# Optimization experiments

Hardware: AMD Instinct MI355X
Metric: run time of the kernel (lower is better)

Reference implementation:

```python
import jax, jax.numpy as jnp
import numpy as np

B, T, D = 4, 4096, 1024
F = 4 * D
EPS_INIT = -1e30  # log-space -inf surrogate for the stable WKV state


def layer_norm(x, w, b, eps=1e-5):
    mu = jnp.mean(x, axis=-1, keepdims=True)
    var = jnp.var(x, axis=-1, keepdims=True)
    return (x - mu) * jax.lax.rsqrt(var + eps) * w + b


def time_shift(x):
    # last_x[t] = x[t-1], zeros at t=0 (init_x buffer is zeros)
    return jnp.concatenate([jnp.zeros_like(x[:, :1]), x[:, :-1]], axis=1)


def wkv(w, u, k, v):
    """Numerically stable RWKV WKV recurrence.
    w, u: [D] (w already exponentiated decay rate); k, v: [B,T,D].
    Maintains (alpha, beta, eps) so that wkv_t = (sum_i e^{k_i - (t-1-i)w} v_i + e^{u+k_t} v_t)
                                               / (sum_i e^{k_i - (t-1-i)w}     + e^{u+k_t})."""
    bsz, _, dim = k.shape
    alpha0 = jnp.zeros((bsz, dim), k.dtype)
    beta0 = jnp.zeros((bsz, dim), k.dtype)
    eps0 = jnp.full((bsz, dim), EPS_INIT, k.dtype)

    def step(carry, kv_t):
        alpha, beta, eps = carry
        kt, vt = kv_t
        ukt = u + kt
        tau = jnp.maximum(ukt, eps)
        e1 = jnp.exp(eps - tau)
        e2 = jnp.exp(ukt - tau)
        out = (e1 * alpha + e2 * vt) / (e1 * beta + e2)
        # decay state by exp(-w) in log-space, then absorb k_t
        weps = eps - w
        tau2 = jnp.maximum(weps, kt)
        d1 = jnp.exp(weps - tau2)
        d2 = jnp.exp(kt - tau2)
        return (d1 * alpha + d2 * vt, d1 * beta + d2, tau2), out

    kT = jnp.swapaxes(k, 0, 1)  # [T,B,D]
    vT = jnp.swapaxes(v, 0, 1)
    _, outT = jax.lax.scan(step, (alpha0, beta0, eps0), (kT, vT))
    return jnp.swapaxes(outT, 0, 1)  # [B,T,D]


def setup_inputs() -> dict:
    key = jax.random.key(0)
    ks = jax.random.split(key, 20)
    n = lambda k, shape, s: jax.random.normal(k, shape, jnp.float32) * s
    u = lambda k, shape: jax.random.uniform(k, shape, jnp.float32)
    s = 0.02
    return {
        "x": jax.random.normal(ks[0], (B, T, D), jnp.float32),
        "ln1_w": jnp.ones((D,), jnp.float32), "ln1_b": jnp.zeros((D,), jnp.float32),
        "ln2_w": jnp.ones((D,), jnp.float32), "ln2_b": jnp.zeros((D,), jnp.float32),
        "time_decay": n(ks[1], (D,), 0.5),
        "time_first": n(ks[2], (D,), 0.5),
        "time_mix_k": u(ks[3], (1, 1, D)),
        "time_mix_v": u(ks[4], (1, 1, D)),
        "time_mix_r": u(ks[5], (1, 1, D)),
        "w_key": n(ks[6], (D, D), s),
        "w_value": n(ks[7], (D, D), s),
        "w_recept": n(ks[8], (D, D), s),
        "w_output": n(ks[9], (D, D), s),
        "f_time_mix_k": u(ks[10], (1, 1, D)),
        "f_time_mix_r": u(ks[11], (1, 1, D)),
        "f_w_key": n(ks[12], (D, F), s),
        "f_w_recept": n(ks[13], (D, D), s),
        "f_w_value": n(ks[14], (F, D), s),
    }


def reference(x, ln1_w, ln1_b, ln2_w, ln2_b,
              time_decay, time_first, time_mix_k, time_mix_v, time_mix_r,
              w_key, w_value, w_recept, w_output,
              f_time_mix_k, f_time_mix_r, f_w_key, f_w_recept, f_w_value):
    # --- attention (time-mix) sub-block ---
    xn = layer_norm(x, ln1_w, ln1_b)
    lx = time_shift(xn)
    k = (xn * time_mix_k + lx * (1.0 - time_mix_k)) @ w_key
    v = (xn * time_mix_v + lx * (1.0 - time_mix_v)) @ w_value
    r = (xn * time_mix_r + lx * (1.0 - time_mix_r)) @ w_recept
    sr = jax.nn.sigmoid(r)
    w = jnp.exp(time_decay)
    out = wkv(w, time_first, k, v)
    x = x + (out * sr) @ w_output
    # --- feed-forward (channel-mix) sub-block ---
    xn2 = layer_norm(x, ln2_w, ln2_b)
    lx2 = time_shift(xn2)
    fk = (xn2 * f_time_mix_k + lx2 * (1.0 - f_time_mix_k)) @ f_w_key
    fr = (xn2 * f_time_mix_r + lx2 * (1.0 - f_time_mix_r)) @ f_w_recept
    vk = jnp.square(jax.nn.relu(fk)) @ f_w_value
    x = x + jax.nn.sigmoid(fr) * vk
    return x
```

## Files before the change

kernel.cpp:

```cpp
#include <hip/hip_runtime.h>

#define DV 1024
#define TT 4096
#define BB 4
#define FF 4096
#define MM (BB*TT)
#define NCH 64
#define LCH 64

typedef __attribute__((ext_vector_type(8))) short bf16x8;
typedef __attribute__((ext_vector_type(4))) float f32x4;
typedef __attribute__((ext_vector_type(8))) unsigned short u16x8;
typedef __attribute__((ext_vector_type(4))) unsigned short u16x4;

__device__ __forceinline__ float bf2f(unsigned short h) {
    union { unsigned int u; float f; } c; c.u = ((unsigned int)h) << 16; return c.f;
}
__device__ __forceinline__ unsigned short f2bf(float f) {
    union { float f; unsigned int u; } c; c.f = f;
    unsigned int r = c.u + 0x7fffu + ((c.u >> 16) & 1u);
    return (unsigned short)(r >> 16);
}

__global__ void diag_kernel(float* out, float v) { out[0] = v; }

__global__ __launch_bounds__(256) void transpose_cast(
    const float* __restrict__ src, unsigned short* __restrict__ dst, int K, int N)
{
    __shared__ float t[32][33];
    int n0 = blockIdx.x * 32, k0 = blockIdx.y * 32;
    int tx = threadIdx.x, ty = threadIdx.y;
    #pragma unroll
    for (int i = 0; i < 4; ++i)
        t[ty*4+i][tx] = src[(size_t)(k0 + ty*4 + i) * N + n0 + tx];
    __syncthreads();
    #pragma unroll
    for (int i = 0; i < 4; ++i)
        dst[(size_t)(n0 + ty*4 + i) * K + k0 + tx] = f2bf(t[tx][ty*4+i]);
}

template<bool BF16IN>
__global__ __launch_bounds__(256) void ln_kernel(
    const void* __restrict__ xin, const float* __restrict__ w, const float* __restrict__ b,
    unsigned short* __restrict__ out)
{
    int row = blockIdx.x;
    int t = threadIdx.x;
    float v0, v1, v2, v3;
    if (BF16IN) {
        u16x4 h = *(const u16x4*)((const unsigned short*)xin + (size_t)row * DV + t * 4);
        v0 = bf2f(h[0]); v1 = bf2f(h[1]); v2 = bf2f(h[2]); v3 = bf2f(h[3]);
    } else {
        float4 v = ((const float4*)((const float*)xin + (size_t)row * DV))[t];
        v0 = v.x; v1 = v.y; v2 = v.z; v3 = v.w;
    }
    float s = v0 + v1 + v2 + v3;
    float q = v0*v0 + v1*v1 + v2*v2 + v3*v3;
    #pragma unroll
    for (int off = 32; off >= 1; off >>= 1) {
        s += __shfl_down(s, off);
        q += __shfl_down(q, off);
    }
    __shared__ float ss[4], qq[4];
    if ((t & 63) == 0) { ss[t >> 6] = s; qq[t >> 6] = q; }
    __syncthreads();
    s = ss[0] + ss[1] + ss[2] + ss[3];
    q = qq[0] + qq[1] + qq[2] + qq[3];
    float mu = s * (1.f/DV);
    float var = q * (1.f/DV) - mu*mu;
    float rs = rsqrtf(var + 1e-5f);
    int d = t * 4;
    u16x4 o;
    o[0] = f2bf((v0 - mu)*rs*w[d+0] + b[d+0]);
    o[1] = f2bf((v1 - mu)*rs*w[d+1] + b[d+1]);
    o[2] = f2bf((v2 - mu)*rs*w[d+2] + b[d+2]);
    o[3] = f2bf((v3 - mu)*rs*w[d+3] + b[d+3]);
    *(u16x4*)(out + (size_t)row*DV + d) = o;
}

__global__ __launch_bounds__(256) void mix_kernel(
    const unsigned short* __restrict__ xn,
    const float* __restrict__ ck, const float* __restrict__ cv, const float* __restrict__ cr,
    unsigned short* __restrict__ ok, unsigned short* __restrict__ ov, unsigned short* __restrict__ orr)
{
    int gid = blockIdx.x * 256 + threadIdx.x;
    int row = gid >> 7;
    int d0 = (gid & 127) << 3;
    size_t base = (size_t)row * DV + d0;
    u16x8 cur = *(const u16x8*)(xn + base);
    bool hp = (row & (TT - 1)) != 0;
    u16x8 prev = (u16x8)0;
    if (hp) prev = *(const u16x8*)(xn + base - DV);
    u16x8 rk, rv, rr2;
    #pragma unroll
    for (int e = 0; e < 8; ++e) {
        float xc = bf2f(cur[e]);
        float xp = hp ? bf2f(prev[e]) : 0.f;
        float a = ck[d0+e]; rk[e] = f2bf(xc*a + xp*(1.f-a));
        float bb = cv[d0+e]; rv[e] = f2bf(xc*bb + xp*(1.f-bb));
        if (orr) { float c = cr[d0+e]; rr2[e] = f2bf(xc*c + xp*(1.f-c)); }
    }
    *(u16x8*)(ok + base) = rk;
    *(u16x8*)(ov + base) = rv;
    if (orr) *(u16x8*)(orr + base) = rr2;
}


__global__ __launch_bounds__(256) void wkv_phase1(
    const unsigned short* __restrict__ k, const unsigned short* __restrict__ v,
    const float* __restrict__ time_decay,
    float* __restrict__ saP, float* __restrict__ sbP, float* __restrict__ mP)
{
    int gid = blockIdx.x * 256 + threadIdx.x;
    int d = gid & (DV - 1);
    int bc = gid >> 10;
    int b = bc >> 6, c = bc & (NCH - 1);
    float w = __expf(time_decay[d]);
    float alpha = 0.f, beta = 0.f, m = -1e30f;
    size_t base = ((size_t)b * TT + (size_t)c * LCH) * DV + d;
    for (int t = 0; t < LCH; ++t) {
        size_t idx = base + (size_t)t * DV;
        float kt = bf2f(k[idx]);
        float vt = bf2f(v[idx]);
        float wm = m - w;
        float tau = fmaxf(wm, kt);
        float d1 = __expf(wm - tau);
        float d2 = __expf(kt - tau);
        alpha = d1*alpha + d2*vt;
        beta  = d1*beta + d2;
        m = tau;
    }
    saP[gid] = alpha; sbP[gid] = beta; mP[gid] = m;
}

__global__ __launch_bounds__(256) void wkv_phase2(
    const float* __restrict__ time_decay,
    float* __restrict__ saP, float* __restrict__ sbP, float* __restrict__ mP)
{
    int gid = blockIdx.x * 256 + threadIdx.x;
    int b = gid >> 10, d = gid & (DV - 1);
    float Lw = (float)LCH * __expf(time_decay[d]);
    float A = 0.f, Bv = 0.f, E = -1e30f;
    for (int c = 0; c < NCH; ++c) {
        int idx = ((b * NCH + c) << 10) + d;
        float sa = saP[idx], sb = sbP[idx], mc = mP[idx];
        saP[idx] = A; sbP[idx] = Bv; mP[idx] = E;
        float de = E - Lw;
        float m2 = fmaxf(de, mc);
        float e1 = __expf(de - m2);
        float e2 = __expf(mc - m2);
        A  = e1*A  + e2*sa;
        Bv = e1*Bv + e2*sb;
        E  = m2;
    }
}

__global__ __launch_bounds__(256) void wkv_phase3(
    const unsigned short* __restrict__ k, const unsigned short* __restrict__ v,
    const unsigned short* __restrict__ r,
    const float* __restrict__ time_decay, const float* __restrict__ time_first,
    const float* __restrict__ saP, const float* __restrict__ sbP, const float* __restrict__ mP,
    unsigned short* __restrict__ aout)
{
    int gid = blockIdx.x * 256 + threadIdx.x;
    int d = gid & (DV - 1);
    int bc = gid >> 10;
    int b = bc >> 6, c = bc & (NCH - 1);
    float w = __expf(time_decay[d]);
    float u = time_first[d];
    float alpha = saP[gid], beta = sbP[gid], eps = mP[gid];
    size_t base = ((size_t)b * TT + (size_t)c * LCH) * DV + d;
    for (int t = 0; t < LCH; ++t) {
        size_t idx = base + (size_t)t * DV;
        float kt = bf2f(k[idx]);
        float vt = bf2f(v[idx]);
        float ukt = u + kt;
        float tau = fmaxf(ukt, eps);
        float e1 = __expf(eps - tau);
        float e2 = __expf(ukt - tau);
        float out = (e1*alpha + e2*vt) / (e1*beta + e2);
        float weps = eps - w;
        float tau2 = fmaxf(weps, kt);
        float d1 = __expf(weps - tau2);
        float d2 = __expf(kt - tau2);
        alpha = d1*alpha + d2*vt;
        beta  = d1*beta + d2;
        eps = tau2;
        float rt = bf2f(r[idx]);
        float sr = 1.f / (1.f + __expf(-rt));
        aout[idx] = f2bf(out * sr);
    }
}

template<int MODE>
__global__ __launch_bounds__(256) void gemm_bf16(
    const short* __restrict__ A, const short* __restrict__ Bt,
    void* __restrict__ Cout, int M, int N, int K,
    const void* __restrict__ res, const unsigned short* __restrict__ gate)
{
    __shared__ short sA[128 * 40];
    __shared__ short sB[128 * 40];
    const int m0 = blockIdx.y * 128, n0 = blockIdx.x * 128;
    const int t = threadIdx.x;
    const int lane = t & 63, wv = t >> 6;
    const int wr = wv >> 1, wc = wv & 1;
    const int lm = lane & 15, lk = (lane >> 4) * 8;
    const int r0 = t >> 2;
    const int r1 = r0 + 64;
    const int c0 = (t & 3) * 8;
    f32x4 acc[4][4] = {};

    for (int k0 = 0; k0 < K; k0 += 32) {
        bf16x8 va0 = *(const bf16x8*)(A  + (size_t)(m0 + r0) * K + k0 + c0);
        bf16x8 va1 = *(const bf16x8*)(A  + (size_t)(m0 + r1) * K + k0 + c0);
        bf16x8 vb0 = *(const bf16x8*)(Bt + (size_t)(n0 + r0) * K + k0 + c0);
        bf16x8 vb1 = *(const bf16x8*)(Bt + (size_t)(n0 + r1) * K + k0 + c0);
        __syncthreads();
        *(bf16x8*)&sA[r0 * 40 + c0] = va0;
        *(bf16x8*)&sA[r1 * 40 + c0] = va1;
        *(bf16x8*)&sB[r0 * 40 + c0] = vb0;
        *(bf16x8*)&sB[r1 * 40 + c0] = vb1;
        __syncthreads();
        bf16x8 af[4], bfr[4];
        #pragma unroll
        for (int i = 0; i < 4; ++i)
            af[i] = *(const bf16x8*)&sA[(wr*64 + i*16 + lm) * 40 + lk];
        #pragma unroll
        for (int j = 0; j < 4; ++j)
            bfr[j] = *(const bf16x8*)&sB[(wc*64 + j*16 + lm) * 40 + lk];
        #pragma unroll
        for (int i = 0; i < 4; ++i)
            #pragma unroll
            for (int j = 0; j < 4; ++j)
                acc[i][j] = __builtin_amdgcn_mfma_f32_16x16x32_bf16(af[i], bfr[j], acc[i][j], 0, 0, 0);
    }

    #pragma unroll
    for (int i = 0; i < 4; ++i)
        #pragma unroll
        for (int j = 0; j < 4; ++j)
            #pragma unroll
            for (int rr = 0; rr < 4; ++rr) {
                int gm = m0 + wr*64 + i*16 + (lane >> 4)*4 + rr;
                int gn = n0 + wc*64 + j*16 + lm;
                size_t off = (size_t)gm * N + gn;
                float val = acc[i][j][rr];
                if (MODE == 1) {
                    ((unsigned short*)Cout)[off] = f2bf(val);
                } else if (MODE == 3) {
                    float rl = fmaxf(val, 0.f);
                    ((unsigned short*)Cout)[off] = f2bf(rl * rl);
                } else if (MODE == 5) {
                    ((unsigned short*)Cout)[off] = f2bf(val + ((const float*)res)[off]);
                } else {
                    float g = bf2f(gate[off]);
                    float sg = 1.f / (1.f + __expf(-g));
                    ((float*)Cout)[off] = bf2f(((const unsigned short*)res)[off]) + sg * val;
                }
            }
}

extern "C" void kernel_launch(void* const* d_in, const int* in_sizes, int n_in,
                              void* d_out, int out_size, void* d_ws, size_t ws_size,
                              hipStream_t stream) {
    const float* x          = (const float*)d_in[0];
    const float* ln1_w      = (const float*)d_in[1];
    const float* ln1_b      = (const float*)d_in[2];
    const float* ln2_w      = (const float*)d_in[3];
    const float* ln2_b      = (const float*)d_in[4];
    const float* time_decay = (const float*)d_in[5];
    const float* time_first = (const float*)d_in[6];
    const float* tmk        = (const float*)d_in[7];
    const float* tmv        = (const float*)d_in[8];
    const float* tmr        = (const float*)d_in[9];
    const float* w_key      = (const float*)d_in[10];
    const float* w_value    = (const float*)d_in[11];
    const float* w_recept   = (const float*)d_in[12];
    const float* w_output   = (const float*)d_in[13];
    const float* f_tmk      = (const float*)d_in[14];
    const float* f_tmr      = (const float*)d_in[15];
    const float* f_w_key    = (const float*)d_in[16];
    const float* f_w_recept = (const float*)d_in[17];
    const float* f_w_value  = (const float*)d_in[18];

    char* ws = (char*)d_ws;
    const size_t MB = 1ull << 20;
    if (ws_size < 160 * MB) {
        diag_kernel<<<1, 1, 0, stream>>>((float*)d_out, (float)ws_size);
        return;
    }

    unsigned short* wkT  = (unsigned short*)(ws + 0*MB);
    unsigned short* wvT  = (unsigned short*)(ws + 2*MB);
    unsigned short* wrT  = (unsigned short*)(ws + 4*MB);
    unsigned short* woT  = (unsigned short*)(ws + 6*MB);
    unsigned short* fwkT = (unsigned short*)(ws + 8*MB);
    unsigned short* fwrT = (unsigned short*)(ws + 16*MB);
    unsigned short* fwvT = (unsigned short*)(ws + 18*MB);
    float* saP = (float*)(ws + 26*MB);
    float* sbP = (float*)(ws + 27*MB);
    float* mP  = (float*)(ws + 28*MB);
    unsigned short* S0 = (unsigned short*)(ws + 32*MB);
    unsigned short* S1 = (unsigned short*)(ws + 64*MB);
    unsigned short* S2 = (unsigned short*)(ws + 96*MB);
    unsigned short* S3 = (unsigned short*)(ws + 128*MB);
    unsigned short* xn    = S0;
    unsigned short* xk    = S1;
    unsigned short* xv    = S2;
    unsigned short* xr    = S3;
    unsigned short* kbuf  = S0;
    unsigned short* vbuf  = S1;
    unsigned short* rbuf  = S2;
    unsigned short* abuf  = S3;
    unsigned short* x1    = S0;
    unsigned short* xn2   = S1;
    unsigned short* fkx   = S2;
    unsigned short* frx   = S3;
    unsigned short* frbuf = S1;
    unsigned short* hk    = S3;

    dim3 tb(32, 8);
    transpose_cast<<<dim3(32, 32),  tb, 0, stream>>>(w_key,      wkT,  1024, 1024);
    transpose_cast<<<dim3(32, 32),  tb, 0, stream>>>(w_value,    wvT,  1024, 1024);
    transpose_cast<<<dim3(32, 32),  tb, 0, stream>>>(w_recept,   wrT,  1024, 1024);
    transpose_cast<<<dim3(32, 32),  tb, 0, stream>>>(w_output,   woT,  1024, 1024);
    transpose_cast<<<dim3(128, 32), tb, 0, stream>>>(f_w_key,    fwkT, 1024, 4096);
    transpose_cast<<<dim3(32, 32),  tb, 0, stream>>>(f_w_recept, fwrT, 1024, 1024);
    transpose_cast<<<dim3(32, 128), tb, 0, stream>>>(f_w_value,  fwvT, 4096, 1024);

    ln_kernel<false><<<MM, 256, 0, stream>>>(x, ln1_w, ln1_b, xn);
    mix_kernel<<<MM*DV/8/256, 256, 0, stream>>>(xn, tmk, tmv, tmr, xk, xv, xr);
    gemm_bf16<1><<<dim3(8, 128), 256, 0, stream>>>((const short*)xk, (const short*)wkT, kbuf, MM, 1024, 1024, nullptr, nullptr);
    gemm_bf16<1><<<dim3(8, 128), 256, 0, stream>>>((const short*)xv, (const short*)wvT, vbuf, MM, 1024, 1024, nullptr, nullptr);
    gemm_bf16<1><<<dim3(8, 128), 256, 0, stream>>>((const short*)xr, (const short*)wrT, rbuf, MM, 1024, 1024, nullptr, nullptr);
    wkv_phase1<<<BB*NCH*DV/256, 256, 0, stream>>>(kbuf, vbuf, time_decay, saP, sbP, mP);
    wkv_phase2<<<BB*DV/256, 256, 0, stream>>>(time_decay, saP, sbP, mP);
    wkv_phase3<<<BB*NCH*DV/256, 256, 0, stream>>>(kbuf, vbuf, rbuf, time_decay, time_first, saP, sbP, mP, abuf);
    gemm_bf16<5><<<dim3(8, 128), 256, 0, stream>>>((const short*)abuf, (const short*)woT, x1, MM, 1024, 1024, x, nullptr);

    ln_kernel<true><<<MM, 256, 0, stream>>>(x1, ln2_w, ln2_b, xn2);
    mix_kernel<<<MM*DV/8/256, 256, 0, stream>>>(xn2, f_tmk, f_tmr, nullptr, fkx, frx, nullptr);
    gemm_bf16<1><<<dim3(8, 128), 256, 0, stream>>>((const short*)frx, (const short*)fwrT, frbuf, MM, 1024, 1024, nullptr, nullptr);
    for (int c = 0; c < 4; ++c) {
        const size_t rows = 4096;
        const size_t aoff = (size_t)c * rows * 1024;
        gemm_bf16<3><<<dim3(32, 32), 256, 0, stream>>>(
            (const short*)(fkx + aoff), (const short*)fwkT, hk, rows, 4096, 1024, nullptr, nullptr);
        gemm_bf16<6><<<dim3(8, 32), 256, 0, stream>>>(
            (const short*)hk, (const short*)fwvT, (float*)d_out + aoff, rows, 1024, 4096,
            x1 + aoff, frbuf + aoff);
    }
}
```

Baseline: 1.338 ms.

## Use direct global-to-LDS loads in GEMM and split FFN by hidden slices

The GEMM tile loads now use global_load_lds to write straight into shared memory, dropping the register round trip and the padded LDS stride. The FFN is restructured so each of four 1024-wide hidden slices runs over all rows, with the value-projection partial sums accumulated into the fp32 output across launches. The gating and residual are applied only on the last slice. The unpadded LDS layout may add bank conflicts on fragment reads, and the accumulation adds extra fp32 read-modify-write traffic on the output.

New measurement: 1.339 ms. Within noise of the previous version (+0.1%).

```diff
diff --git a/kernel.cpp b/kernel.cpp
--- a/kernel.cpp
+++ b/kernel.cpp
@@ -20,6 +20,12 @@
     union { float f; unsigned int u; } c; c.f = f;
     unsigned int r = c.u + 0x7fffu + ((c.u >> 16) & 1u);
     return (unsigned short)(r >> 16);
+}
+
+__device__ __forceinline__ void gl16(const void* g, void* l) {
+    __builtin_amdgcn_global_load_lds(
+        (const __attribute__((address_space(1))) void*)g,
+        (__attribute__((address_space(3))) void*)l, 16, 0, 0);
 }
 
 __global__ void diag_kernel(float* out, float v) { out[0] = v; }
@@ -104,7 +110,6 @@
     *(u16x8*)(ov + base) = rv;
     if (orr) *(u16x8*)(orr + base) = rr2;
 }
-
 
 __global__ __launch_bounds__(256) void wkv_phase1(
     const unsigned short* __restrict__ k, const unsigned short* __restrict__ v,
@@ -198,36 +203,34 @@
     void* __restrict__ Cout, int M, int N, int K,
     const void* __restrict__ res, const unsigned short* __restrict__ gate)
 {
-    __shared__ short sA[128 * 40];
-    __shared__ short sB[128 * 40];
+    __shared__ short sA[128 * 32];
+    __shared__ short sB[128 * 32];
     const int m0 = blockIdx.y * 128, n0 = blockIdx.x * 128;
     const int t = threadIdx.x;
     const int lane = t & 63, wv = t >> 6;
     const int wr = wv >> 1, wc = wv & 1;
     const int lm = lane & 15, lk = (lane >> 4) * 8;
-    const int r0 = t >> 2;
-    const int r1 = r0 + 64;
-    const int c0 = (t & 3) * 8;
+    const int srow = lane >> 2;
+    const int scol = (lane & 3) * 8;
     f32x4 acc[4][4] = {};
 
     for (int k0 = 0; k0 < K; k0 += 32) {
-        bf16x8 va0 = *(const bf16x8*)(A  + (size_t)(m0 + r0) * K + k0 + c0);
-        bf16x8 va1 = *(const bf16x8*)(A  + (size_t)(m0 + r1) * K + k0 + c0);
-        bf16x8 vb0 = *(const bf16x8*)(Bt + (size_t)(n0 + r0) * K + k0 + c0);
-        bf16x8 vb1 = *(const bf16x8*)(Bt + (size_t)(n0 + r1) * K + k0 + c0);
         __syncthreads();
-        *(bf16x8*)&sA[r0 * 40 + c0] = va0;
-        *(bf16x8*)&sA[r1 * 40 + c0] = va1;
-        *(bf16x8*)&sB[r0 * 40 + c0] = vb0;
-        *(bf16x8*)&sB[r1 * 40 + c0] = vb1;
+        #pragma unroll
+        for (int i = 0; i < 2; ++i) {
+            int c = wv + i * 4;
+            int row = c * 16 + srow;
+            gl16(A  + (size_t)(m0 + row) * K + k0 + scol, sA + c * 512);
+            gl16(Bt + (size_t)(n0 + row) * K + k0 + scol, sB + c * 512);
+        }
         __syncthreads();
         bf16x8 af[4], bfr[4];
         #pragma unroll
         for (int i = 0; i < 4; ++i)
-            af[i] = *(const bf16x8*)&sA[(wr*64 + i*16 + lm) * 40 + lk];
+            af[i] = *(const bf16x8*)&sA[(wr*64 + i*16 + lm) * 32 + lk];
         #pragma unroll
         for (int j = 0; j < 4; ++j)
-            bfr[j] = *(const bf16x8*)&sB[(wc*64 + j*16 + lm) * 40 + lk];
+            bfr[j] = *(const bf16x8*)&sB[(wc*64 + j*16 + lm) * 32 + lk];
         #pragma unroll
         for (int i = 0; i < 4; ++i)
             #pragma unroll
@@ -252,10 +255,15 @@
                     ((unsigned short*)Cout)[off] = f2bf(rl * rl);
                 } else if (MODE == 5) {
                     ((unsigned short*)Cout)[off] = f2bf(val + ((const float*)res)[off]);
+                } else if (MODE == 7) {
+                    ((float*)Cout)[off] = val;
+                } else if (MODE == 8) {
+                    ((float*)Cout)[off] += val;
                 } else {
                     float g = bf2f(gate[off]);
                     float sg = 1.f / (1.f + __expf(-g));
-                    ((float*)Cout)[off] = bf2f(((const unsigned short*)res)[off]) + sg * val;
+                    float sum = ((float*)Cout)[off] + val;
+                    ((float*)Cout)[off] = bf2f(((const unsigned short*)res)[off]) + sg * sum;
                 }
             }
 }
@@ -317,7 +325,7 @@
     unsigned short* fkx   = S2;
     unsigned short* frx   = S3;
     unsigned short* frbuf = S1;
-    unsigned short* hk    = S3;
+    unsigned short* hkf   = S3;
 
     dim3 tb(32, 8);
     transpose_cast<<<dim3(32, 32),  tb, 0, stream>>>(w_key,      wkT,  1024, 1024);
@@ -326,7 +334,9 @@
     transpose_cast<<<dim3(32, 32),  tb, 0, stream>>>(w_output,   woT,  1024, 1024);
     transpose_cast<<<dim3(128, 32), tb, 0, stream>>>(f_w_key,    fwkT, 1024, 4096);
     transpose_cast<<<dim3(32, 32),  tb, 0, stream>>>(f_w_recept, fwrT, 1024, 1024);
-    transpose_cast<<<dim3(32, 128), tb, 0, stream>>>(f_w_value,  fwvT, 4096, 1024);
+    for (int f = 0; f < 4; ++f)
+        transpose_cast<<<dim3(32, 32), tb, 0, stream>>>(
+            f_w_value + (size_t)f * 1024 * 1024, fwvT + (size_t)f * 1024 * 1024, 1024, 1024);
 
     ln_kernel<false><<<MM, 256, 0, stream>>>(x, ln1_w, ln1_b, xn);
     mix_kernel<<<MM*DV/8/256, 256, 0, stream>>>(xn, tmk, tmv, tmr, xk, xv, xr);
@@ -341,13 +351,15 @@
     ln_kernel<true><<<MM, 256, 0, stream>>>(x1, ln2_w, ln2_b, xn2);
     mix_kernel<<<MM*DV/8/256, 256, 0, stream>>>(xn2, f_tmk, f_tmr, nullptr, fkx, frx, nullptr);
     gemm_bf16<1><<<dim3(8, 128), 256, 0, stream>>>((const short*)frx, (const short*)fwrT, frbuf, MM, 1024, 1024, nullptr, nullptr);
-    for (int c = 0; c < 4; ++c) {
-        const size_t rows = 4096;
-        const size_t aoff = (size_t)c * rows * 1024;
-        gemm_bf16<3><<<dim3(32, 32), 256, 0, stream>>>(
-            (const short*)(fkx + aoff), (const short*)fwkT, hk, rows, 4096, 1024, nullptr, nullptr);
-        gemm_bf16<6><<<dim3(8, 32), 256, 0, stream>>>(
-            (const short*)hk, (const short*)fwvT, (float*)d_out + aoff, rows, 1024, 4096,
-            x1 + aoff, frbuf + aoff);
-    }
-}
+    for (int f = 0; f < 4; ++f) {
+        const short* fwk_f = (const short*)(fwkT + (size_t)f * 1024 * 1024);
+        const short* fwv_f = (const short*)(fwvT + (size_t)f * 1024 * 1024);
+        gemm_bf16<3><<<dim3(8, 128), 256, 0, stream>>>((const short*)fkx, fwk_f, hkf, MM, 1024, 1024, nullptr, nullptr);
+        if (f == 0)
+            gemm_bf16<7><<<dim3(8, 128), 256, 0, stream>>>((const short*)hkf, fwv_f, (float*)d_out, MM, 1024, 1024, nullptr, nullptr);
+        else if (f < 3)
+            gemm_bf16<8><<<dim3(8, 128), 256, 0, stream>>>((const short*)hkf, fwv_f, (float*)d_out, MM, 1024, 1024, nullptr, nullptr);
+        else
+            gemm_bf16<9><<<dim3(8, 128), 256, 0, stream>>>((const short*)hkf, fwv_f, (float*)d_out, MM, 1024, 1024, x1, frbuf);
+    }
+}
```
